# Kernel optimization log

Measured on AMD Instinct MI355X. Metric: run time of the kernel, lower is better.

Reference implementation:

```python
import jax, jax.numpy as jnp
import numpy as np

B = 256  # number of graphs in the batch


def _gcn(x, W, b, src, dst):
    """PyG GCNConv: self-loops + symmetric deg normalization. x:[N,Fin], W:[Fin,Fout]."""
    n = x.shape[0]
    h = x @ W  # [N, Fout]
    deg = jax.ops.segment_sum(jnp.ones(src.shape[0], h.dtype), dst, num_segments=n) + 1.0  # +1 self-loop
    norm = jax.lax.rsqrt(deg)  # [N]
    agg = jax.ops.segment_sum(h[src] * norm[src, None], dst, num_segments=n)  # gather-scale-scatter
    return norm[:, None] * (agg + norm[:, None] * h) + b  # self-loop term norm_i^2 * h_i


def _gep(x, batch):
    """Global mean pool per graph."""
    s = jax.ops.segment_sum(x, batch, num_segments=B)
    c = jax.ops.segment_sum(jnp.ones(x.shape[0], x.dtype), batch, num_segments=B)
    return s / jnp.maximum(c, 1.0)[:, None]


def _branch(x, edge_index, batch, w1, b1, w2, b2, w3, b3, fw1, fb1, fw2, fb2):
    src, dst = edge_index[0], edge_index[1]
    x = jax.nn.relu(_gcn(x, w1, b1, src, dst))
    x = jax.nn.relu(_gcn(x, w2, b2, src, dst))
    x = jax.nn.relu(_gcn(x, w3, b3, src, dst))
    x = _gep(x, batch)  # [B, 4*F]
    x = jax.nn.relu(x @ fw1 + fb1)
    x = x @ fw2 + fb2  # dropout = identity in eval
    return x


def setup_inputs() -> dict:
    key = jax.random.key(0)
    ks = iter(jax.random.split(key, 40))
    N_MOL, E_MOL, F_MOL = 10240, 40960, 78
    N_PRO, E_PRO, F_PRO = 76800, 768000, 54
    OUT_DIM = 128

    def p(shape):
        return jax.random.normal(next(ks), shape, jnp.float32) * 0.05

    inp = {}
    inp['mol_x'] = jax.random.normal(next(ks), (N_MOL, F_MOL), jnp.float32)
    inp['mol_edge_index'] = jax.random.randint(next(ks), (2, E_MOL), 0, N_MOL)
    inp['mol_batch'] = jnp.sort(jax.random.randint(next(ks), (N_MOL,), 0, B))
    inp['pro_x'] = jax.random.normal(next(ks), (N_PRO, F_PRO), jnp.float32)
    inp['pro_edge_index'] = jax.random.randint(next(ks), (2, E_PRO), 0, N_PRO)
    inp['pro_batch'] = jnp.sort(jax.random.randint(next(ks), (N_PRO,), 0, B))

    # molecule branch params
    inp['mw1'], inp['mb1'] = p((F_MOL, F_MOL)), p((F_MOL,))
    inp['mw2'], inp['mb2'] = p((F_MOL, 2 * F_MOL)), p((2 * F_MOL,))
    inp['mw3'], inp['mb3'] = p((2 * F_MOL, 4 * F_MOL)), p((4 * F_MOL,))
    inp['mfw1'], inp['mfb1'] = p((4 * F_MOL, 1024)), p((1024,))
    inp['mfw2'], inp['mfb2'] = p((1024, OUT_DIM)), p((OUT_DIM,))
    # protein branch params
    inp['pw1'], inp['pb1'] = p((F_PRO, F_PRO)), p((F_PRO,))
    inp['pw2'], inp['pb2'] = p((F_PRO, 2 * F_PRO)), p((2 * F_PRO,))
    inp['pw3'], inp['pb3'] = p((2 * F_PRO, 4 * F_PRO)), p((4 * F_PRO,))
    inp['pfw1'], inp['pfb1'] = p((4 * F_PRO, 1024)), p((1024,))
    inp['pfw2'], inp['pfb2'] = p((1024, OUT_DIM)), p((OUT_DIM,))
    # combined head
    inp['fc1w'], inp['fc1b'] = p((2 * OUT_DIM, 1024)), p((1024,))
    inp['fc2w'], inp['fc2b'] = p((1024, 512)), p((512,))
    inp['outw'], inp['outb'] = p((512, 1)), p((1,))
    return inp


def reference(mol_x, mol_edge_index, mol_batch, pro_x, pro_edge_index, pro_batch,
              mw1, mb1, mw2, mb2, mw3, mb3, mfw1, mfb1, mfw2, mfb2,
              pw1, pb1, pw2, pb2, pw3, pb3, pfw1, pfb1, pfw2, pfb2,
              fc1w, fc1b, fc2w, fc2b, outw, outb):
    xm = _branch(mol_x, mol_edge_index, mol_batch, mw1, mb1, mw2, mb2, mw3, mb3, mfw1, mfb1, mfw2, mfb2)
    xp = _branch(pro_x, pro_edge_index, pro_batch, pw1, pb1, pw2, pb2, pw3, pb3, pfw1, pfb1, pfw2, pfb2)
    xc = jnp.concatenate([xm, xp], axis=1)  # [B, 256]
    xc = jax.nn.relu(xc @ fc1w + fc1b)
    xc = jax.nn.relu(xc @ fc2w + fc2b)
    return xc @ outw + outb  # [B, 1]
```

## Files before the change

### kernel.cpp

```cpp
#include <hip/hip_runtime.h>


static inline int cdiv(int a, int b) { return (a + b - 1) / b; }


__device__ __forceinline__ unsigned short f2bf(float x) {
    unsigned u = __float_as_uint(x);
    u += 0x7FFFu + ((u >> 16) & 1u);
    return (unsigned short)(u >> 16);
}
__device__ __forceinline__ float bf2f(unsigned short h) {
    return __uint_as_float((unsigned)h << 16);
}


__global__ void deg2_kernel(const int* __restrict__ dstA, int* __restrict__ degA, int EA,
                            const int* __restrict__ dstB, int* __restrict__ degB, int EB) {
    int t = blockIdx.x * blockDim.x + threadIdx.x;
    if (t < EA) { atomicAdd(&degA[dstA[t]], 1); return; }
    t -= EA;
    if (t < EB) atomicAdd(&degB[dstB[t]], 1);
}

__global__ void degsum2_kernel(const int* __restrict__ deg_p, int NP, int nbp,
                               const int* __restrict__ deg_m, int NM, int* __restrict__ bsum) {
    __shared__ int s[256];
    int b = blockIdx.x, tid = threadIdx.x;
    const int* deg; int N, bi;
    if (b < nbp) { deg = deg_p; N = NP; bi = b; }
    else         { deg = deg_m; N = NM; bi = b - nbp; }
    int t = bi * 256 + tid;
    s[tid] = (t < N) ? deg[t] : 0;
    __syncthreads();
    for (int off = 128; off > 0; off >>= 1) {
        if (tid < off) s[tid] += s[tid + off];
        __syncthreads();
    }
    if (tid == 0) bsum[b] = s[0];
}

__global__ void scan2_kernel(int* __restrict__ bsum, int nbp, int nbm) {
    __shared__ int s[512];
    int tid = threadIdx.x;
    int total = nbp + nbm;
    int v = (tid < total) ? bsum[tid] : 0;
    bool isMol = (tid >= nbp);
    s[tid] = v;
    __syncthreads();
    for (int off = 1; off < 512; off <<= 1) {
        int x = 0;
        if (tid >= off) {
            int src = tid - off;
            if ((src >= nbp) == isMol) x = s[src];
        }
        __syncthreads();
        s[tid] += x;
        __syncthreads();
    }
    if (tid < total) bsum[tid] = s[tid] - v;
}

__global__ void alloc_scan2_kernel(const int* __restrict__ deg_p, int* rs_p, int* fc_p, float* n_p,
                                   int NP, int nbp,
                                   const int* __restrict__ deg_m, int* rs_m, int* fc_m, float* n_m,
                                   int NM, const int* __restrict__ bsum) {
    __shared__ int s[256];
    int b = blockIdx.x, tid = threadIdx.x;
    const int* deg; int* rs; int* fc; float* nrm; int N, bi;
    if (b < nbp) { deg = deg_p; rs = rs_p; fc = fc_p; nrm = n_p; N = NP; bi = b; }
    else         { deg = deg_m; rs = rs_m; fc = fc_m; nrm = n_m; N = NM; bi = b - nbp; }
    int t = bi * 256 + tid;
    int v = (t < N) ? deg[t] : 0;
    s[tid] = v;
    __syncthreads();
    for (int off = 1; off < 256; off <<= 1) {
        int x = (tid >= off) ? s[tid - off] : 0;
        __syncthreads();
        s[tid] += x;
        __syncthreads();
    }
    if (t < N) {
        int start = bsum[b] + s[tid] - v;
        rs[t] = start;
        fc[t] = start;
        nrm[t] = rsqrtf((float)v + 1.0f);
    }
}

__global__ void fill2_kernel(const int* srcA, const int* dstA, int* fcA, int* esA, int EA,
                             const int* srcB, const int* dstB, int* fcB, int* esB, int EB) {
    int t = blockIdx.x * blockDim.x + threadIdx.x;
    if (t < EA) { int p = atomicAdd(&fcA[dstA[t]], 1); esA[p] = srcA[t]; return; }
    t -= EA;
    if (t < EB) { int p = atomicAdd(&fcB[dstB[t]], 1); esB[p] = srcB[t]; }
}

__device__ __forceinline__ void gs_body(const int* batch, int* gs, int t, int N, int B) {
    int b = batch[t];
    int bp = (t == 0) ? -1 : batch[t - 1];
    for (int g = bp + 1; g <= b; ++g) gs[g] = t;
    if (t == N - 1) for (int g = b + 1; g <= B; ++g) gs[g] = N;
}

__global__ void gs2_kernel(const int* batchA, int* gsA, int NA,
                           const int* batchB, int* gsB, int NB, int B) {
    int t = blockIdx.x * blockDim.x + threadIdx.x;
    if (t < NA) { gs_body(batchA, gsA, t, NA, B); return; }
    t -= NA;
    if (t < NB) gs_body(batchB, gsB, t, NB, B);
}

__global__ void pad2_kernel(const float* xA, float* yA, int NA, int FA, int SA,
                            const float* xB, float* yB, int NB, int FB, int SB) {
    int t = blockIdx.x * blockDim.x + threadIdx.x;
    if (t < NA * SA) {
        int r = t / SA, j = t - r * SA;
        yA[t] = (j < FA) ? xA[(size_t)r * FA + j] : 0.0f;
        return;
    }
    t -= NA * SA;
    if (t < NB * SB) {
        int r = t / SB, j = t - r * SB;
        yB[t] = (j < FB) ? xB[(size_t)r * FB + j] : 0.0f;
    }
}


__global__ void wpack_kernel(
    const float* __restrict__ w1p, const float* __restrict__ w2p, const float* __restrict__ w3p,
    const float* __restrict__ b1p, const float* __restrict__ b2p, const float* __restrict__ b3p,
    const float* __restrict__ w1m, const float* __restrict__ w2m, const float* __restrict__ w3m,
    const float* __restrict__ b1m, const float* __restrict__ b2m, const float* __restrict__ b3m,
    unsigned short* __restrict__ Wh, unsigned short* __restrict__ Wl, float* __restrict__ Bp)
{
    int t = blockIdx.x * 256 + threadIdx.x;
    if (t < 143360) {
        const float* w; int Kp, K, N, off;
        if      (t <  4096) { w = w1p; Kp = 64;  K = 54;  N = 54;  off = 0; }
        else if (t < 12288) { w = w2p; Kp = 64;  K = 54;  N = 108; off = 4096; }
        else if (t < 45056) { w = w3p; Kp = 128; K = 108; N = 216; off = 12288; }
        else if (t < 57344) { w = w1m; Kp = 96;  K = 78;  N = 78;  off = 45056; }
        else if (t < 81920) { w = w2m; Kp = 128; K = 78;  N = 156; off = 57344; }
        else                { w = w3m; Kp = 192; K = 156; N = 312; off = 81920; }
        int local = t - off;
        int n = local / Kp, k = local - n * Kp;
        float v = (k < K && n < N) ? w[(size_t)k * N + n] : 0.0f;
        unsigned short h = f2bf(v);
        Wh[t] = h;
        Wl[t] = f2bf(v - bf2f(h));
        return;
    }
    int u = t - 143360;
    if (u < 1088) {
        const float* b; int N, off;
        if      (u <  64) { b = b1p; N = 54;  off = 0; }
        else if (u < 192) { b = b2p; N = 108; off = 64; }
        else if (u < 448) { b = b3p; N = 216; off = 192; }
        else if (u < 576) { b = b1m; N = 78;  off = 448; }
        else if (u < 768) { b = b2m; N = 156; off = 576; }
        else              { b = b3m; N = 312; off = 768; }
        int n = u - off;
        Bp[u] = (n < N) ? b[n] : 0.0f;
    }
}


__device__ __forceinline__ float4 vmad(float s, float4 a, float4 b) {
    return make_float4(fmaf(s, a.x, b.x), fmaf(s, a.y, b.y), fmaf(s, a.z, b.z), fmaf(s, a.w, b.w));
}
__device__ __forceinline__ float4 vmul(float s, float4 a) {
    return make_float4(s * a.x, s * a.y, s * a.z, s * a.w);
}
__device__ __forceinline__ ushort4 bfsplit_h(float4 a) {
    ushort4 h; h.x = f2bf(a.x); h.y = f2bf(a.y); h.z = f2bf(a.z); h.w = f2bf(a.w); return h;
}
__device__ __forceinline__ ushort4 bfsplit_l(float4 a, ushort4 h) {
    ushort4 l;
    l.x = f2bf(a.x - bf2f(h.x)); l.y = f2bf(a.y - bf2f(h.y));
    l.z = f2bf(a.z - bf2f(h.z)); l.w = f2bf(a.w - bf2f(h.w));
    return l;
}


typedef __attribute__((ext_vector_type(8))) short s16x8;
typedef __attribute__((ext_vector_type(4))) float f32x4_t;

template <int KP, int NPo>
__device__ __forceinline__ void fused_body(
    const float* __restrict__ X, const float* __restrict__ norm,
    const int* __restrict__ rs, const int* __restrict__ deg, const int* __restrict__ es,
    const unsigned short* __restrict__ Wh, const unsigned short* __restrict__ Wl,
    const float* __restrict__ bias, float* __restrict__ out,
    int brow, unsigned short* Ah, unsigned short* Al)
{
    constexpr int LDK = KP + 8;
    constexpr int FV  = KP / 4;
    constexpr int FV2 = FV / 2;
    constexpr int NF  = NPo / 64;
    const int tid = threadIdx.x;

    const float4* xv = reinterpret_cast<const float4*>(X);
    for (int p = tid; p < 64 * FV2; p += 256) {
        int r = p / FV2, q = p - r * FV2;
        int n = brow + r;
        size_t base = (size_t)n * FV;
        float4 a0 = vmul(norm[n], xv[base + q]);
        float4 a1 = vmul(norm[n], xv[base + q + FV2]);
        int rsv = rs[n], d = deg[n];
        const int* e = es + rsv;
        int i = 0;
        for (; i + 4 <= d; i += 4) {
            int s0 = e[i], s1 = e[i + 1], s2 = e[i + 2], s3 = e[i + 3];
            float n0 = norm[s0], n1 = norm[s1], n2 = norm[s2], n3 = norm[s3];
            size_t b0 = (size_t)s0 * FV, b1 = (size_t)s1 * FV;
            size_t b2 = (size_t)s2 * FV, b3 = (size_t)s3 * FV;
            float4 v00 = xv[b0 + q], v01 = xv[b0 + q + FV2];
            float4 v10 = xv[b1 + q], v11 = xv[b1 + q + FV2];
            float4 v20 = xv[b2 + q], v21 = xv[b2 + q + FV2];
            float4 v30 = xv[b3 + q], v31 = xv[b3 + q + FV2];
            a0 = vmad(n0, v00, a0); a1 = vmad(n0, v01, a1);
            a0 = vmad(n1, v10, a0); a1 = vmad(n1, v11, a1);
            a0 = vmad(n2, v20, a0); a1 = vmad(n2, v21, a1);
            a0 = vmad(n3, v30, a0); a1 = vmad(n3, v31, a1);
        }
        for (; i < d; ++i) {
            int s0 = e[i];
            float n0 = norm[s0];
            size_t b0 = (size_t)s0 * FV;
            a0 = vmad(n0, xv[b0 + q], a0);
            a1 = vmad(n0, xv[b0 + q + FV2], a1);
        }
        ushort4 h0 = bfsplit_h(a0), l0 = bfsplit_l(a0, h0);
        ushort4 h1 = bfsplit_h(a1), l1 = bfsplit_l(a1, h1);
        *reinterpret_cast<ushort4*>(&Ah[r * LDK + 4 * q]) = h0;
        *reinterpret_cast<ushort4*>(&Ah[r * LDK + 4 * (q + FV2)]) = h1;
        *reinterpret_cast<ushort4*>(&Al[r * LDK + 4 * q]) = l0;
        *reinterpret_cast<ushort4*>(&Al[r * LDK + 4 * (q + FV2)]) = l1;
    }
    __syncthreads();

    const int wave = tid >> 6, lane = tid & 63;
    const int l15 = lane & 15, l4 = lane >> 4;
    const int nc0 = wave * (NPo / 4);

    f32x4_t acc[4][NF];
#pragma unroll
    for (int mf = 0; mf < 4; ++mf)
#pragma unroll
        for (int nf = 0; nf < NF; ++nf)
            acc[mf][nf] = (f32x4_t){0.f, 0.f, 0.f, 0.f};

    for (int k0 = 0; k0 < KP; k0 += 32) {
        s16x8 ah[4], al[4];
#pragma unroll
        for (int mf = 0; mf < 4; ++mf) {
            int r = mf * 16 + l15;
            ah[mf] = *reinterpret_cast<const s16x8*>(&Ah[r * LDK + k0 + l4 * 8]);
            al[mf] = *reinterpret_cast<const s16x8*>(&Al[r * LDK + k0 + l4 * 8]);
        }
#pragma unroll
        for (int nf = 0; nf < NF; ++nf) {
            size_t wb = (size_t)(nc0 + nf * 16 + l15) * KP + k0 + l4 * 8;
            s16x8 bh = *reinterpret_cast<const s16x8*>(&Wh[wb]);
            s16x8 bl = *reinterpret_cast<const s16x8*>(&Wl[wb]);
#pragma unroll
            for (int mf = 0; mf < 4; ++mf) {
                acc[mf][nf] = __builtin_amdgcn_mfma_f32_16x16x32_bf16(ah[mf], bh, acc[mf][nf], 0, 0, 0);
                acc[mf][nf] = __builtin_amdgcn_mfma_f32_16x16x32_bf16(ah[mf], bl, acc[mf][nf], 0, 0, 0);
                acc[mf][nf] = __builtin_amdgcn_mfma_f32_16x16x32_bf16(al[mf], bh, acc[mf][nf], 0, 0, 0);
            }
        }
    }

#pragma unroll
    for (int mf = 0; mf < 4; ++mf) {
#pragma unroll
        for (int reg = 0; reg < 4; ++reg) {
            int gm = brow + mf * 16 + l4 * 4 + reg;
            float sc = norm[gm];
#pragma unroll
            for (int nf = 0; nf < NF; ++nf) {
                int gn = nc0 + nf * 16 + l15;
                out[(size_t)gm * NPo + gn] = fmaxf(fmaf(sc, acc[mf][nf][reg], bias[gn]), 0.f);
            }
        }
    }
}

template <int KPA, int NPA, int KPB, int NPB>
__global__ __launch_bounds__(256) void fused_gcn2_kernel(
    const float* XA, const float* nA, const int* rsA, const int* dA, const int* esA,
    const unsigned short* WhA, const unsigned short* WlA, const float* bsA, float* oA, int nbA,
    const float* XB, const float* nB, const int* rsB, const int* dB, const int* esB,
    const unsigned short* WhB, const unsigned short* WlB, const float* bsB, float* oB)
{
    constexpr int KMAX = (KPA > KPB ? KPA : KPB);
    __shared__ __align__(16) unsigned short Ah[64 * (KMAX + 8)];
    __shared__ __align__(16) unsigned short Al[64 * (KMAX + 8)];
    int bid = blockIdx.x;
    if (bid < nbA)
        fused_body<KPA, NPA>(XA, nA, rsA, dA, esA, WhA, WlA, bsA, oA, bid * 64, Ah, Al);
    else
        fused_body<KPB, NPB>(XB, nB, rsB, dB, esB, WhB, WlB, bsB, oB, (bid - nbA) * 64, Ah, Al);
}


template <bool RELU, int MR, int JT>
__device__ __forceinline__ void fc_body(
    const float* __restrict__ X, const float* __restrict__ W,
    const float* __restrict__ bias, float* __restrict__ out,
    int K, int N, int out_stride, int out_off, int bx, int by, float* smem)
{
    constexpr int TJ = JT / 4;
    constexpr int SK = 256 / TJ;
    float* Xs = smem;
    float* red = smem + MR * K;

    const int tid = threadIdx.x;
    const int m0 = by * MR;
    const int j0 = bx * JT;

    for (int idx = tid; idx < MR * K; idx += 256) {
        int r = idx / K, k = idx - r * K;
        Xs[idx] = X[(size_t)(m0 + r) * K + k];
    }
    __syncthreads();

    const int tj = tid % TJ;
    const int s  = tid / TJ;
    const int chunk = (K + SK - 1) / SK;
    const int kb = s * chunk;
    const int ke = min(K, kb + chunk);

    const float4* w4 = reinterpret_cast<const float4*>(W + j0) + tj;
    const int wstride = N >> 2;

    float4 acc[MR];
#pragma unroll
    for (int r = 0; r < MR; ++r) acc[r] = make_float4(0.f, 0.f, 0.f, 0.f);
    for (int k = kb; k < ke; ++k) {
        float4 w = w4[(size_t)k * wstride];
#pragma unroll
        for (int r = 0; r < MR; ++r)
            acc[r] = vmad(Xs[r * K + k], w, acc[r]);
    }
#pragma unroll
    for (int r = 0; r < MR; ++r) {
        float* rr = red + ((s * MR + r) * JT) + tj * 4;
        rr[0] = acc[r].x; rr[1] = acc[r].y; rr[2] = acc[r].z; rr[3] = acc[r].w;
    }
    __syncthreads();

    for (int o = tid; o < MR * JT; o += 256) {
        int r = o / JT, j = o - r * JT;
        float v = 0.f;
#pragma unroll
        for (int ss = 0; ss < SK; ++ss) v += red[(ss * MR + r) * JT + j];
        v += bias[j0 + j];
        if (RELU) v = fmaxf(v, 0.0f);
        out[(size_t)(m0 + r) * out_stride + out_off + j0 + j] = v;
    }
}

template <bool RELU, int MR, int JT>
__global__ __launch_bounds__(256) void fc2_kernel(
    const float* XA, const float* WA, const float* bA, float* oA,
    int KA, int NA, int osA, int ooA, int nbA, int gxA,
    const float* XB, const float* WB, const float* bB, float* oB,
    int KB, int NB, int osB, int ooB, int gxB)
{
    extern __shared__ float smem[];
    int bid = blockIdx.x;
    if (bid < nbA) {
        fc_body<RELU, MR, JT>(XA, WA, bA, oA, KA, NA, osA, ooA, bid % gxA, bid / gxA, smem);
    } else {
        bid -= nbA;
        fc_body<RELU, MR, JT>(XB, WB, bB, oB, KB, NB, osB, ooB, bid % gxB, bid / gxB, smem);
    }
}

template <bool RELU, int MR, int JT>
__global__ __launch_bounds__(256) void fc_kernel(
    const float* X, const float* W, const float* b, float* o,
    int K, int N, int out_stride, int out_off)
{
    extern __shared__ float smem[];
    fc_body<RELU, MR, JT>(X, W, b, o, K, N, out_stride, out_off, blockIdx.x, blockIdx.y, smem);
}

__global__ __launch_bounds__(256) void matvec_kernel(
    const float* __restrict__ X, const float* __restrict__ W,
    const float* __restrict__ bias, float* __restrict__ out, int K)
{
    __shared__ float red[256];
    const int m = blockIdx.x;
    const int tid = threadIdx.x;
    float acc = 0.f;
    for (int k = tid; k < K; k += 256) acc = fmaf(X[(size_t)m * K + k], W[k], acc);
    red[tid] = acc;
    __syncthreads();
    for (int w = 128; w >= 64; w >>= 1) {
        if (tid < w) red[tid] += red[tid + w];
        __syncthreads();
    }
    if (tid < 64) {
        float v = red[tid];
        for (int off = 32; off > 0; off >>= 1) v += __shfl_down(v, off, 64);
        if (tid == 0) out[m] = v + bias[0];
    }
}


__global__ __launch_bounds__(1024) void pool3_kernel(
    const float* __restrict__ xA, const int* __restrict__ gsA, float* __restrict__ poolA,
    const float* __restrict__ xB, const int* __restrict__ gsB, float* __restrict__ poolB)
{
    __shared__ float4 red[1024];
    const int b = blockIdx.x, tid = threadIdx.x;
    const float4* xv; const int* gs; float* pool; int Fv, sv, g;
    if (b < 256) { xv = (const float4*)xA; gs = gsA; pool = poolA; Fv = 54; sv = 64; g = b; }
    else         { xv = (const float4*)xB; gs = gsB; pool = poolB; Fv = 78; sv = 80; g = b - 256; }
    const int s = gs[g], c = gs[g + 1] - s;
    const int nrg = 1024 / Fv;
    const int jv = tid % Fv, rg = tid / Fv;

    float4 acc = make_float4(0.f, 0.f, 0.f, 0.f);
    if (rg < nrg) {
        for (int i = rg; i < c; i += nrg) {
            float4 v = xv[(size_t)(s + i) * sv + jv];
            acc.x += v.x; acc.y += v.y; acc.z += v.z; acc.w += v.w;
        }
    }
    red[tid] = acc;
    __syncthreads();
    if (rg == 0) {
        for (int q = 1; q < nrg; ++q) {
            float4 v = red[q * Fv + jv];
            acc.x += v.x; acc.y += v.y; acc.z += v.z; acc.w += v.w;
        }
        const float fc_ = (float)max(c, 1);
        float4 o = make_float4(acc.x / fc_, acc.y / fc_, acc.z / fc_, acc.w / fc_);
        *reinterpret_cast<float4*>(&pool[(size_t)g * (Fv * 4) + jv * 4]) = o;
    }
}

extern "C" void kernel_launch(void* const* d_in, const int* in_sizes, int n_in,
                              void* d_out, int out_size, void* d_ws, size_t ws_size,
                              hipStream_t stream) {
    const float* mol_x     = (const float*)d_in[0];
    const int*   mol_ei    = (const int*)  d_in[1];
    const int*   mol_batch = (const int*)  d_in[2];
    const float* pro_x     = (const float*)d_in[3];
    const int*   pro_ei    = (const int*)  d_in[4];
    const int*   pro_batch = (const int*)  d_in[5];
    const float* mw1 = (const float*)d_in[6],  * mb1 = (const float*)d_in[7];
    const float* mw2 = (const float*)d_in[8],  * mb2 = (const float*)d_in[9];
    const float* mw3 = (const float*)d_in[10], * mb3 = (const float*)d_in[11];
    const float* mfw1 = (const float*)d_in[12], * mfb1 = (const float*)d_in[13];
    const float* mfw2 = (const float*)d_in[14], * mfb2 = (const float*)d_in[15];
    const float* pw1 = (const float*)d_in[16], * pb1 = (const float*)d_in[17];
    const float* pw2 = (const float*)d_in[18], * pb2 = (const float*)d_in[19];
    const float* pw3 = (const float*)d_in[20], * pb3 = (const float*)d_in[21];
    const float* pfw1 = (const float*)d_in[22], * pfb1 = (const float*)d_in[23];
    const float* pfw2 = (const float*)d_in[24], * pfb2 = (const float*)d_in[25];
    const float* fc1w = (const float*)d_in[26], * fc1b = (const float*)d_in[27];
    const float* fc2w = (const float*)d_in[28], * fc2b = (const float*)d_in[29];
    const float* outw = (const float*)d_in[30], * outb = (const float*)d_in[31];
    float* out = (float*)d_out;

    const int NP = 76800, EP = 768000;
    const int NM = 10240, EM = 40960;
    const int NBP = cdiv(NP, 256), NBM = cdiv(NM, 256);

    float* Pp = (float*)d_ws;
    float* Rp = Pp + (size_t)76800 * 256;
    float* Pm = Rp + (size_t)76800 * 128;
    float* Rm = Pm + (size_t)10240 * 320;
    unsigned short* WpkH = (unsigned short*)(Rm + (size_t)10240 * 192);
    unsigned short* WpkL = WpkH + 143360;
    float* Bpk    = (float*)(WpkL + 143360);
    float* norm_p = Bpk + 1088;
    float* norm_m = norm_p + NP;
    float* pool_p = norm_m + NM;
    float* pool_m = pool_p + 256 * 216;
    float* fcb_p  = pool_m + 256 * 312;
    float* fcb_m  = fcb_p + 256 * 1024;
    float* xc     = fcb_m + 256 * 1024;
    float* hb1    = xc + 256 * 256;
    float* hb2    = hb1 + 256 * 1024;
    int* ibase    = (int*)(hb2 + 256 * 512);
    int* deg_p = ibase;
    int* deg_m = deg_p + NP;
    int* rs_p  = deg_m + NM;
    int* fc_p  = rs_p + NP;
    int* es_p  = fc_p + NP;
    int* rs_m  = es_p + EP;
    int* fc_m  = rs_m + NM;
    int* es_m  = fc_m + NM;
    int* gs_p  = es_m + EM;
    int* gs_m  = gs_p + 260;
    int* bsum  = gs_m + 260;

    const int BLK = 256;

    hipMemsetAsync(deg_p, 0, (size_t)(NP + NM) * sizeof(int), stream);
    deg2_kernel<<<cdiv(EP + EM, BLK), BLK, 0, stream>>>(pro_ei + EP, deg_p, EP, mol_ei + EM, deg_m, EM);
    degsum2_kernel<<<NBP + NBM, 256, 0, stream>>>(deg_p, NP, NBP, deg_m, NM, bsum);
    scan2_kernel<<<1, 512, 0, stream>>>(bsum, NBP, NBM);
    alloc_scan2_kernel<<<NBP + NBM, 256, 0, stream>>>(deg_p, rs_p, fc_p, norm_p, NP, NBP,
                                                      deg_m, rs_m, fc_m, norm_m, NM, bsum);
    fill2_kernel<<<cdiv(EP + EM, BLK), BLK, 0, stream>>>(pro_ei, pro_ei + EP, fc_p, es_p, EP,
                                                         mol_ei, mol_ei + EM, fc_m, es_m, EM);
    gs2_kernel<<<cdiv(NP + NM, BLK), BLK, 0, stream>>>(pro_batch, gs_p, NP, mol_batch, gs_m, NM, 256);
    pad2_kernel<<<cdiv(NP * 64 + NM * 96, BLK), BLK, 0, stream>>>(pro_x, Rp, NP, 54, 64,
                                                                  mol_x, Rm, NM, 78, 96);
    wpack_kernel<<<cdiv(143360 + 1088, 256), 256, 0, stream>>>(
        pw1, pw2, pw3, pb1, pb2, pb3, mw1, mw2, mw3, mb1, mb2, mb3, WpkH, WpkL, Bpk);

    const int NB_P = NP / 64;
    const int NB_M = NM / 64;

    fused_gcn2_kernel<64, 64, 96, 128><<<NB_P + NB_M, 256, 0, stream>>>(
        Rp, norm_p, rs_p, deg_p, es_p, WpkH + 0, WpkL + 0, Bpk + 0, Pp, NB_P,
        Rm, norm_m, rs_m, deg_m, es_m, WpkH + 45056, WpkL + 45056, Bpk + 448, Pm);
    fused_gcn2_kernel<64, 128, 128, 192><<<NB_P + NB_M, 256, 0, stream>>>(
        Pp, norm_p, rs_p, deg_p, es_p, WpkH + 4096, WpkL + 4096, Bpk + 64, Rp, NB_P,
        Pm, norm_m, rs_m, deg_m, es_m, WpkH + 57344, WpkL + 57344, Bpk + 576, Rm);
    fused_gcn2_kernel<128, 256, 192, 320><<<NB_P + NB_M, 256, 0, stream>>>(
        Rp, norm_p, rs_p, deg_p, es_p, WpkH + 12288, WpkL + 12288, Bpk + 192, Pp, NB_P,
        Rm, norm_m, rs_m, deg_m, es_m, WpkH + 81920, WpkL + 81920, Bpk + 768, Pm);

    pool3_kernel<<<512, 1024, 0, stream>>>(Pp, gs_p, pool_p, Pm, gs_m, pool_m);

    {
        int gxA = 1024 / 64, nbA = gxA * (256 / 4);
        int gxB = 1024 / 64, nbB = gxB * (256 / 4);
        size_t lds = (size_t)(4 * 312 + 16 * 4 * 64) * sizeof(float);
        fc2_kernel<true, 4, 64><<<nbA + nbB, 256, lds, stream>>>(
            pool_p, pfw1, pfb1, fcb_p, 216, 1024, 1024, 0, nbA, gxA,
            pool_m, mfw1, mfb1, fcb_m, 312, 1024, 1024, 0, gxB);
    }
    {
        int gxA = 128 / 32, nbA = gxA * (256 / 2);
        int gxB = gxA, nbB = nbA;
        size_t lds = (size_t)(2 * 1024 + 32 * 2 * 32) * sizeof(float);
        fc2_kernel<false, 2, 32><<<nbA + nbB, 256, lds, stream>>>(
            fcb_p, pfw2, pfb2, xc, 1024, 128, 256, 128, nbA, gxA,
            fcb_m, mfw2, mfb2, xc, 1024, 128, 256, 0, gxB);
    }

    {
        dim3 grid(1024 / 64, 256 / 4);
        size_t lds = (size_t)(4 * 256 + 16 * 4 * 64) * sizeof(float);
        fc_kernel<true, 4, 64><<<grid, 256, lds, stream>>>(xc, fc1w, fc1b, hb1, 256, 1024, 1024, 0);
    }
    {
        dim3 grid(512 / 64, 256 / 4);
        size_t lds = (size_t)(4 * 1024 + 16 * 4 * 64) * sizeof(float);
        fc_kernel<true, 4, 64><<<grid, 256, lds, stream>>>(hb1, fc2w, fc2b, hb2, 1024, 512, 512, 0);
    }
    matvec_kernel<<<256, 256, 0, stream>>>(hb2, outw, outb, out, 512);
}
```

Baseline: 526.2 us.

## Store GCN activations at tight feature strides and zero-fill K padding in LDS

Intermediate node feature buffers now use strides close to the real feature counts (56/80, 108/156, 216/312) instead of padding up to the MFMA K size. The fused gather kernel reads one float4 per thread slot over the narrower stride and zero-fills the K-padding region in shared memory before the MFMA stage. The mol-branch K padding for layers 2 and 3 also shrinks (128 to 96, 192 to 160), which removes some MFMA work. The goal is to cut gather and store bandwidth in this memory-bound aggregation. In exchange, output stores need a bounds guard, and rows at odd strides such as 27 or 39 float4s lose their alignment to wider cache lines.

```diff
diff --git a/kernel.cpp b/kernel.cpp
--- a/kernel.cpp
+++ b/kernel.cpp
@@ -134,14 +134,14 @@
     unsigned short* __restrict__ Wh, unsigned short* __restrict__ Wl, float* __restrict__ Bp)
 {
     int t = blockIdx.x * 256 + threadIdx.x;
-    if (t < 143360) {
+    if (t < 126976) {
         const float* w; int Kp, K, N, off;
         if      (t <  4096) { w = w1p; Kp = 64;  K = 54;  N = 54;  off = 0; }
         else if (t < 12288) { w = w2p; Kp = 64;  K = 54;  N = 108; off = 4096; }
         else if (t < 45056) { w = w3p; Kp = 128; K = 108; N = 216; off = 12288; }
         else if (t < 57344) { w = w1m; Kp = 96;  K = 78;  N = 78;  off = 45056; }
-        else if (t < 81920) { w = w2m; Kp = 128; K = 78;  N = 156; off = 57344; }
-        else                { w = w3m; Kp = 192; K = 156; N = 312; off = 81920; }
+        else if (t < 75776) { w = w2m; Kp = 96;  K = 78;  N = 156; off = 57344; }
+        else                { w = w3m; Kp = 160; K = 156; N = 312; off = 75776; }
         int local = t - off;
         int n = local / Kp, k = local - n * Kp;
         float v = (k < K && n < N) ? w[(size_t)k * N + n] : 0.0f;
@@ -150,7 +150,7 @@
         Wl[t] = f2bf(v - bf2f(h));
         return;
     }
-    int u = t - 143360;
+    int u = t - 126976;
     if (u < 1088) {
         const float* b; int N, off;
         if      (u <  64) { b = b1p; N = 54;  off = 0; }
@@ -185,7 +185,7 @@
 typedef __attribute__((ext_vector_type(8))) short s16x8;
 typedef __attribute__((ext_vector_type(4))) float f32x4_t;
 
-template <int KP, int NPo>
+template <int KP, int NPo, int FVIN, int NST>
 __device__ __forceinline__ void fused_body(
     const float* __restrict__ X, const float* __restrict__ norm,
     const int* __restrict__ rs, const int* __restrict__ deg, const int* __restrict__ es,
@@ -194,48 +194,45 @@
     int brow, unsigned short* Ah, unsigned short* Al)
 {
     constexpr int LDK = KP + 8;
-    constexpr int FV  = KP / 4;
-    constexpr int FV2 = FV / 2;
     constexpr int NF  = NPo / 64;
+    constexpr int CF  = (KP - 4 * FVIN) / 4;
     const int tid = threadIdx.x;
 
     const float4* xv = reinterpret_cast<const float4*>(X);
-    for (int p = tid; p < 64 * FV2; p += 256) {
-        int r = p / FV2, q = p - r * FV2;
+    for (int p = tid; p < 64 * FVIN; p += 256) {
+        int r = p / FVIN, q = p - r * FVIN;
         int n = brow + r;
-        size_t base = (size_t)n * FV;
-        float4 a0 = vmul(norm[n], xv[base + q]);
-        float4 a1 = vmul(norm[n], xv[base + q + FV2]);
+        float4 a0 = vmul(norm[n], xv[(size_t)n * FVIN + q]);
         int rsv = rs[n], d = deg[n];
         const int* e = es + rsv;
         int i = 0;
         for (; i + 4 <= d; i += 4) {
             int s0 = e[i], s1 = e[i + 1], s2 = e[i + 2], s3 = e[i + 3];
             float n0 = norm[s0], n1 = norm[s1], n2 = norm[s2], n3 = norm[s3];
-            size_t b0 = (size_t)s0 * FV, b1 = (size_t)s1 * FV;
-            size_t b2 = (size_t)s2 * FV, b3 = (size_t)s3 * FV;
-            float4 v00 = xv[b0 + q], v01 = xv[b0 + q + FV2];
-            float4 v10 = xv[b1 + q], v11 = xv[b1 + q + FV2];
-            float4 v20 = xv[b2 + q], v21 = xv[b2 + q + FV2];
-            float4 v30 = xv[b3 + q], v31 = xv[b3 + q + FV2];
-            a0 = vmad(n0, v00, a0); a1 = vmad(n0, v01, a1);
-            a0 = vmad(n1, v10, a0); a1 = vmad(n1, v11, a1);
-            a0 = vmad(n2, v20, a0); a1 = vmad(n2, v21, a1);
-            a0 = vmad(n3, v30, a0); a1 = vmad(n3, v31, a1);
+            float4 v0 = xv[(size_t)s0 * FVIN + q];
+            float4 v1 = xv[(size_t)s1 * FVIN + q];
+            float4 v2 = xv[(size_t)s2 * FVIN + q];
+            float4 v3 = xv[(size_t)s3 * FVIN + q];
+            a0 = vmad(n0, v0, a0);
+            a0 = vmad(n1, v1, a0);
+            a0 = vmad(n2, v2, a0);
+            a0 = vmad(n3, v3, a0);
         }
         for (; i < d; ++i) {
             int s0 = e[i];
-            float n0 = norm[s0];
-            size_t b0 = (size_t)s0 * FV;
-            a0 = vmad(n0, xv[b0 + q], a0);
-            a1 = vmad(n0, xv[b0 + q + FV2], a1);
+            a0 = vmad(norm[s0], xv[(size_t)s0 * FVIN + q], a0);
         }
         ushort4 h0 = bfsplit_h(a0), l0 = bfsplit_l(a0, h0);
-        ushort4 h1 = bfsplit_h(a1), l1 = bfsplit_l(a1, h1);
         *reinterpret_cast<ushort4*>(&Ah[r * LDK + 4 * q]) = h0;
-        *reinterpret_cast<ushort4*>(&Ah[r * LDK + 4 * (q + FV2)]) = h1;
         *reinterpret_cast<ushort4*>(&Al[r * LDK + 4 * q]) = l0;
-        *reinterpret_cast<ushort4*>(&Al[r * LDK + 4 * (q + FV2)]) = l1;
+    }
+    if (CF > 0) {
+        const ushort4 z = {0, 0, 0, 0};
+        for (int u = tid; u < 64 * CF; u += 256) {
+            int r = u / CF, j = u - r * CF;
+            *reinterpret_cast<ushort4*>(&Ah[r * LDK + 4 * FVIN + 4 * j]) = z;
+            *reinterpret_cast<ushort4*>(&Al[r * LDK + 4 * FVIN + 4 * j]) = z;
+        }
     }
     __syncthreads();
 
@@ -281,13 +278,14 @@
 #pragma unroll
             for (int nf = 0; nf < NF; ++nf) {
                 int gn = nc0 + nf * 16 + l15;
-                out[(size_t)gm * NPo + gn] = fmaxf(fmaf(sc, acc[mf][nf][reg], bias[gn]), 0.f);
+                if (gn < NST)
+                    out[(size_t)gm * NST + gn] = fmaxf(fmaf(sc, acc[mf][nf][reg], bias[gn]), 0.f);
             }
         }
     }
 }
 
-template <int KPA, int NPA, int KPB, int NPB>
+template <int KPA, int NPA, int FVA, int NSTA, int KPB, int NPB, int FVB, int NSTB>
 __global__ __launch_bounds__(256) void fused_gcn2_kernel(
     const float* XA, const float* nA, const int* rsA, const int* dA, const int* esA,
     const unsigned short* WhA, const unsigned short* WlA, const float* bsA, float* oA, int nbA,
@@ -299,9 +297,9 @@
     __shared__ __align__(16) unsigned short Al[64 * (KMAX + 8)];
     int bid = blockIdx.x;
     if (bid < nbA)
-        fused_body<KPA, NPA>(XA, nA, rsA, dA, esA, WhA, WlA, bsA, oA, bid * 64, Ah, Al);
+        fused_body<KPA, NPA, FVA, NSTA>(XA, nA, rsA, dA, esA, WhA, WlA, bsA, oA, bid * 64, Ah, Al);
     else
-        fused_body<KPB, NPB>(XB, nB, rsB, dB, esB, WhB, WlB, bsB, oB, (bid - nbA) * 64, Ah, Al);
+        fused_body<KPB, NPB, FVB, NSTB>(XB, nB, rsB, dB, esB, WhB, WlB, bsB, oB, (bid - nbA) * 64, Ah, Al);
 }
 
 
@@ -418,8 +416,8 @@
     __shared__ float4 red[1024];
     const int b = blockIdx.x, tid = threadIdx.x;
     const float4* xv; const int* gs; float* pool; int Fv, sv, g;
-    if (b < 256) { xv = (const float4*)xA; gs = gsA; pool = poolA; Fv = 54; sv = 64; g = b; }
-    else         { xv = (const float4*)xB; gs = gsB; pool = poolB; Fv = 78; sv = 80; g = b - 256; }
+    if (b < 256) { xv = (const float4*)xA; gs = gsA; pool = poolA; Fv = 54; sv = 54; g = b; }
+    else         { xv = (const float4*)xB; gs = gsB; pool = poolB; Fv = 78; sv = 78; g = b - 256; }
     const int s = gs[g], c = gs[g + 1] - s;
     const int nrg = 1024 / Fv;
     const int jv = tid % Fv, rg = tid / Fv;
@@ -473,12 +471,12 @@
     const int NBP = cdiv(NP, 256), NBM = cdiv(NM, 256);
 
     float* Pp = (float*)d_ws;
-    float* Rp = Pp + (size_t)76800 * 256;
-    float* Pm = Rp + (size_t)76800 * 128;
-    float* Rm = Pm + (size_t)10240 * 320;
-    unsigned short* WpkH = (unsigned short*)(Rm + (size_t)10240 * 192);
-    unsigned short* WpkL = WpkH + 143360;
-    float* Bpk    = (float*)(WpkL + 143360);
+    float* Rp = Pp + (size_t)76800 * 216;
+    float* Pm = Rp + (size_t)76800 * 108;
+    float* Rm = Pm + (size_t)10240 * 312;
+    unsigned short* WpkH = (unsigned short*)(Rm + (size_t)10240 * 156);
+    unsigned short* WpkL = WpkH + 126976;
+    float* Bpk    = (float*)(WpkL + 126976);
     float* norm_p = Bpk + 1088;
     float* norm_m = norm_p + NP;
     float* pool_p = norm_m + NM;
@@ -512,23 +510,23 @@
     fill2_kernel<<<cdiv(EP + EM, BLK), BLK, 0, stream>>>(pro_ei, pro_ei + EP, fc_p, es_p, EP,
                                                          mol_ei, mol_ei + EM, fc_m, es_m, EM);
     gs2_kernel<<<cdiv(NP + NM, BLK), BLK, 0, stream>>>(pro_batch, gs_p, NP, mol_batch, gs_m, NM, 256);
-    pad2_kernel<<<cdiv(NP * 64 + NM * 96, BLK), BLK, 0, stream>>>(pro_x, Rp, NP, 54, 64,
-                                                                  mol_x, Rm, NM, 78, 96);
-    wpack_kernel<<<cdiv(143360 + 1088, 256), 256, 0, stream>>>(
+    pad2_kernel<<<cdiv(NP * 56 + NM * 80, BLK), BLK, 0, stream>>>(pro_x, Rp, NP, 54, 56,
+                                                                  mol_x, Rm, NM, 78, 80);
+    wpack_kernel<<<cdiv(126976 + 1088, 256), 256, 0, stream>>>(
         pw1, pw2, pw3, pb1, pb2, pb3, mw1, mw2, mw3, mb1, mb2, mb3, WpkH, WpkL, Bpk);
 
     const int NB_P = NP / 64;
     const int NB_M = NM / 64;
 
-    fused_gcn2_kernel<64, 64, 96, 128><<<NB_P + NB_M, 256, 0, stream>>>(
+    fused_gcn2_kernel<64, 64, 14, 56, 96, 128, 20, 80><<<NB_P + NB_M, 256, 0, stream>>>(
         Rp, norm_p, rs_p, deg_p, es_p, WpkH + 0, WpkL + 0, Bpk + 0, Pp, NB_P,
         Rm, norm_m, rs_m, deg_m, es_m, WpkH + 45056, WpkL + 45056, Bpk + 448, Pm);
-    fused_gcn2_kernel<64, 128, 128, 192><<<NB_P + NB_M, 256, 0, stream>>>(
+    fused_gcn2_kernel<64, 128, 14, 108, 96, 192, 20, 156><<<NB_P + NB_M, 256, 0, stream>>>(
         Pp, norm_p, rs_p, deg_p, es_p, WpkH + 4096, WpkL + 4096, Bpk + 64, Rp, NB_P,
         Pm, norm_m, rs_m, deg_m, es_m, WpkH + 57344, WpkL + 57344, Bpk + 576, Rm);
-    fused_gcn2_kernel<128, 256, 192, 320><<<NB_P + NB_M, 256, 0, stream>>>(
+    fused_gcn2_kernel<128, 256, 27, 216, 160, 320, 39, 312><<<NB_P + NB_M, 256, 0, stream>>>(
         Rp, norm_p, rs_p, deg_p, es_p, WpkH + 12288, WpkL + 12288, Bpk + 192, Pp, NB_P,
-        Rm, norm_m, rs_m, deg_m, es_m, WpkH + 81920, WpkL + 81920, Bpk + 768, Pm);
+        Rm, norm_m, rs_m, deg_m, es_m, WpkH + 75776, WpkL + 75776, Bpk + 768, Pm);
 
     pool3_kernel<<<512, 1024, 0, stream>>>(Pp, gs_p, pool_p, Pm, gs_m, pool_m);
 
```

Measured after the change: 596.9 us. 1.13x slower.
